# Performance work log

Hardware: AMD Instinct MI355X
Metric: run time of the kernel (lower is better)

Reference implementation:

```python
import jax, jax.numpy as jnp
import numpy as np

B, T, C, H = 256, 256, 384, 6
HS = C // H        # 64 head size
P = int(C * 0.8)   # 307 pca_dim
EPS = 1e-6


def _rmsnorm(x, scale):
    rms = jnp.sqrt(jnp.mean(x * x, axis=-1, keepdims=True) + EPS)
    return x / rms * scale


def _orth(W):
    # torch.svd returns V (not V^T); u @ v.t() == u @ vt
    u, _, vt = jnp.linalg.svd(W, full_matrices=False)
    return u @ vt


def setup_inputs() -> dict:
    key = jax.random.key(0)
    ks = jax.random.split(key, 16)
    s = 0.02
    inp = {
        'x': jax.random.normal(ks[0], (B, T, C), jnp.float32),
        'Wq': jax.random.normal(ks[1], (H, C, HS), jnp.float32) * s,
        'Wk': jax.random.normal(ks[2], (H, C, HS), jnp.float32) * s,
        'Wv': jax.random.normal(ks[3], (H, C, HS), jnp.float32) * s,
        'Wp': jax.random.normal(ks[4], (H * HS, C), jnp.float32) * s,
        'bp': jnp.zeros((C,), jnp.float32),
        'scale1': jnp.ones((C,), jnp.float32),
        'scale2': jnp.ones((C,), jnp.float32),
        'W1': jax.random.normal(ks[5], (C, P), jnp.float32) * s,
        'b1': jnp.zeros((P,), jnp.float32),
        'W2': jax.random.normal(ks[6], (P, C), jnp.float32) * s,
        'b2': jnp.zeros((C,), jnp.float32),
        'Wo_in': jax.random.normal(ks[7], (C, C), jnp.float32),
        'Wo_out': jax.random.normal(ks[8], (C, C), jnp.float32),
    }
    return inp


def reference(x, Wq, Wk, Wv, Wp, bp, scale1, scale2, W1, b1, W2, b2, Wo_in, Wo_out):
    # ln1
    h = _rmsnorm(x, scale1)                                   # [B,T,C]
    # multi-head causal self-attention (heads batched via einsum)
    q = jnp.einsum('btc,hcd->bhtd', h, Wq)                    # [B,H,T,HS]
    k = jnp.einsum('btc,hcd->bhtd', h, Wk)
    v = jnp.einsum('btc,hcd->bhtd', h, Wv)
    wei = jnp.einsum('bhtd,bhsd->bhts', q, k) * (HS ** -0.5)  # [B,H,T,T]
    causal = jnp.tril(jnp.ones((T, T), bool))
    wei = jnp.where(causal, wei, -jnp.inf)
    wei = jax.nn.softmax(wei, axis=-1)
    attn = jnp.einsum('bhts,bhsd->bhtd', wei, v)              # [B,H,T,HS]
    attn = attn.transpose(0, 2, 1, 3).reshape(B, T, H * HS)   # concat heads
    h = attn @ Wp + bp + h                                    # residual on ln1 output
    # ln2
    h = _rmsnorm(h, scale2)
    # input orthogonal transform
    h = h @ _orth(Wo_in)
    # PCA feed-forward (dropout = identity in eval)
    h = jax.nn.relu(h @ W1 + b1)
    h = h @ W2 + b2
    # output orthogonal transform + residual on ff output
    out = h @ _orth(Wo_out) + h
    return out
```

## Files before the change

### kernel.cpp

```cpp
#include <hip/hip_runtime.h>

typedef unsigned short u16;
typedef unsigned int   u32;
typedef short s16x8 __attribute__((ext_vector_type(8)));
typedef float f32x4 __attribute__((ext_vector_type(4)));

static __device__ __forceinline__ float bf2f(u16 v){ return __uint_as_float(((u32)v)<<16); }
static __device__ __forceinline__ u16 f2bf(float f){
  u32 u = __float_as_uint(f);
  u32 r = (u + 0x7fffu + ((u>>16)&1u)) >> 16;
  return (u16)r;
}
static __device__ __forceinline__ float cvt(float v){ return v; }
static __device__ __forceinline__ float cvt(u16 v){ return bf2f(v); }
static __device__ __forceinline__ void stv(float* p, float v){ *p = v; }
static __device__ __forceinline__ void stv(u16* p, float v){ *p = f2bf(v); }

static __device__ __forceinline__ void ld2(const float* p, float& a, float& b){
  float2 t = *(const float2*)p; a=t.x; b=t.y;
}
static __device__ __forceinline__ void ld2(const u16* p, float& a, float& b){
  u32 t = *(const u32*)p; a = __uint_as_float(t<<16); b = __uint_as_float(t & 0xffff0000u);
}
static __device__ __forceinline__ void st2(float* p, float a, float b){
  float2 t; t.x=a; t.y=b; *(float2*)p = t;
}
static __device__ __forceinline__ void st2(u16* p, float a, float b){
  *(u32*)p = ((u32)f2bf(a)) | (((u32)f2bf(b))<<16);
}

template<typename TI, typename TO>
__global__ __launch_bounds__(256) void rms_k(const TI* __restrict__ X,
                                             const float* __restrict__ scale,
                                             TO* __restrict__ O)
{
  int row = blockIdx.x*4 + (threadIdx.x>>6);
  int lane = threadIdx.x&63;
  const TI* xr = X + (size_t)row*384;
  float v[6]; float ss = 0.f;
#pragma unroll
  for(int i=0;i<3;i++){
    ld2(xr + 2*lane + 128*i, v[2*i], v[2*i+1]);
    ss += v[2*i]*v[2*i] + v[2*i+1]*v[2*i+1];
  }
#pragma unroll
  for(int off=32; off>0; off>>=1) ss += __shfl_down(ss, off, 64);
  ss = __shfl(ss, 0, 64);
  float r = rsqrtf(ss*(1.0f/384.0f)+1e-6f);
  TO* orow = O + (size_t)row*384;
#pragma unroll
  for(int i=0;i<3;i++){
    int c = 2*lane + 128*i;
    st2(orow + c, v[2*i]*r*scale[c], v[2*i+1]*r*scale[c+1]);
  }
}

__global__ __launch_bounds__(256) void tcast_k(const float* __restrict__ In, long isz,
                                               u16* __restrict__ Out, long osz,
                                               int Rr, int Cc, int ldo)
{
  __shared__ float t[32][33];
  const int z = blockIdx.z;
  const float* I = In + (long)z*isz;
  u16* Oz = Out + (long)z*osz;
  const int r0 = blockIdx.x*32, c0 = blockIdx.y*32;
  const int tx = threadIdx.x&31, ty = threadIdx.x>>5;
#pragma unroll
  for(int rr=ty; rr<32; rr+=8){
    int r = r0+rr, c = c0+tx;
    t[rr][tx] = (r<Rr && c<Cc) ? I[(size_t)r*Cc + c] : 0.f;
  }
  __syncthreads();
#pragma unroll
  for(int cc=ty; cc<32; cc+=8){
    int c = c0+cc, r = r0+tx;
    if(c<Cc && r<ldo) Oz[(size_t)c*ldo + r] = f2bf(t[tx][cc]);
  }
}

template<int NF, typename TC, typename TR>
__global__ __launch_bounds__(256,2) void mgemmN_k(
    const u16* __restrict__ A, int lda,
    const u16* __restrict__ Bt, int ldb,
    TC* __restrict__ C, long cs_hi, int cs_lo, int csz,
    const TR* __restrict__ R,
    const float* __restrict__ bias,
    int N, int Nstore, int K, float beta, int relu, int nby)
{
  constexpr int BN = NF*32;
  __shared__ __align__(16) u16 As[128*40];
  __shared__ __align__(16) u16 Bs[BN*40];
  const int d = blockIdx.x;
  const int xcd = d&7, slot = d>>3;
  const int bm = xcd*64 + slot/nby;
  const int bn = slot - (slot/nby)*nby;
  const int m0 = bm*128, n0 = bn*BN;
  const int tid = threadIdx.x;
  const int w = tid>>6, lane = tid&63;
  const int g4 = lane>>4, l16 = lane&15;
  const int wr = w>>1, wc = w&1;
  const int arow = tid>>1, akc = (tid&1)*16;

  f32x4 fz = {0.f,0.f,0.f,0.f};
  f32x4 acc[4][NF];
#pragma unroll
  for(int i=0;i<4;i++)
#pragma unroll
    for(int j=0;j<NF;j++) acc[i][j]=fz;

  for(int k0=0;k0<K;k0+=32){
    {
      const u16* ga = &A[(size_t)(m0+arow)*lda + k0 + akc];
      uint4 a0 = *(const uint4*)ga;
      uint4 a1 = *(const uint4*)(ga+8);
      *(uint4*)&As[arow*40 + akc]     = a0;
      *(uint4*)&As[arow*40 + akc + 8] = a1;
    }
#pragma unroll
    for(int j=0;j<(BN+127)/128;j++){
      int brow = (tid>>1) + 128*j;
      if(brow < BN){
        int gn = n0 + brow;
        uint4 b0 = make_uint4(0,0,0,0), b1 = b0;
        if(gn < N){
          const u16* gb = &Bt[(size_t)gn*ldb + k0 + akc];
          b0 = *(const uint4*)gb;
          b1 = *(const uint4*)(gb+8);
        }
        *(uint4*)&Bs[brow*40 + akc]     = b0;
        *(uint4*)&Bs[brow*40 + akc + 8] = b1;
      }
    }
    __syncthreads();
    s16x8 av[4];
#pragma unroll
    for(int mf=0;mf<4;mf++)
      av[mf] = *(const s16x8*)&As[(wr*64 + mf*16 + l16)*40 + g4*8];
#pragma unroll
    for(int nf=0;nf<NF;nf++){
      s16x8 bv = *(const s16x8*)&Bs[(wc*(NF*16) + nf*16 + l16)*40 + g4*8];
#pragma unroll
      for(int mf=0;mf<4;mf++)
        acc[mf][nf] = __builtin_amdgcn_mfma_f32_16x16x32_bf16(av[mf], bv, acc[mf][nf], 0,0,0);
    }
    __syncthreads();
  }
#pragma unroll
  for(int mf=0;mf<4;mf++)
#pragma unroll
    for(int i=0;i<4;i++){
      int m = m0 + wr*64 + mf*16 + g4*4 + i;
      long rowoff = (long)(m>>8)*cs_hi + (long)(m&255)*cs_lo;
#pragma unroll
      for(int nf=0;nf<NF;nf++){
        int gn = n0 + wc*(NF*16) + nf*16 + l16;
        if(gn < Nstore){
          long addr = rowoff + (long)(gn>>6)*csz + (gn&63);
          float v = 0.f;
          if(gn < N){
            v = acc[mf][nf][i];
            if(R)    v += beta*cvt(R[addr]);
            if(bias) v += bias[gn];
            if(relu) v  = fmaxf(v, 0.f);
          }
          stv(C + addr, v);
        }
      }
    }
}

__global__ __launch_bounds__(256,2) void mattn_k(const u16* __restrict__ QKV,
                                                 u16* __restrict__ O)
{
  __shared__ __align__(16) u16 Ks[64*64];
  __shared__ __align__(16) u16 Vts[64*64];
  __shared__ __align__(16) u16 Ps[4*4096];
  const int bh = blockIdx.x;
  const int b = bh/6, h = bh - b*6;
  const u16* Qb = QKV + (size_t)bh*49152;
  const u16* Kb = Qb + 16384;
  const u16* Vb = Qb + 32768;
  const int tid = threadIdx.x;
  const int w = tid>>6, lane = tid&63;
  const int g4 = lane>>4, l16 = lane&15;
  char* PB = (char*)&Ps[w*4096];
  const int swz = (l16&7)<<4;

  s16x8 qf[4][2];
#pragma unroll
  for(int mi=0;mi<4;mi++)
#pragma unroll
    for(int ks=0;ks<2;ks++)
      qf[mi][ks] = *(const s16x8*)(Qb + (size_t)(w*64 + mi*16 + l16)*64 + ks*32 + g4*8);

  f32x4 fzv = {0.f,0.f,0.f,0.f};
  f32x4 o[4][4];
#pragma unroll
  for(int mf=0;mf<4;mf++)
#pragma unroll
    for(int df=0;df<4;df++) o[mf][df]=fzv;
  float mrun[4], lrun[4];
#pragma unroll
  for(int mi=0;mi<4;mi++){ mrun[mi]=-1e30f; lrun[mi]=0.f; }

  for(int st=0; st<4; ++st){
    if(st) __syncthreads();
#pragma unroll
    for(int it=0; it<2; ++it){
      int c = tid + 256*it;
      int s = c>>3, d0 = (c&7)*8;
      uint4 ld = *(const uint4*)(Kb + (size_t)(st*64+s)*64 + d0);
      int byte = s*128 + d0*2; byte ^= (s&7)<<4;
      *(uint4*)((char*)Ks + byte) = ld;
    }
#pragma unroll
    for(int it=0; it<2; ++it){
      int c = tid + 256*it;
      int s = c&63, d0 = (c>>6)*8;
      uint4 ld = *(const uint4*)(Vb + (size_t)(st*64+s)*64 + d0);
#pragma unroll
      for(int jj=0; jj<4; ++jj){
        u32 ww = (jj==0)?ld.x:(jj==1)?ld.y:(jj==2)?ld.z:ld.w;
        int d = d0 + 2*jj;
        int byte0 = d*128 + s*2;     byte0 ^= (d&7)<<4;
        int byte1 = (d+1)*128 + s*2; byte1 ^= ((d+1)&7)<<4;
        *(u16*)((char*)Vts + byte0) = (u16)(ww & 0xffffu);
        *(u16*)((char*)Vts + byte1) = (u16)(ww >> 16);
      }
    }
    __syncthreads();
    if(w < st) continue;

    f32x4 sc[4][4];
#pragma unroll
    for(int sf=0; sf<4; ++sf){
      int row = sf*16 + l16;
      s16x8 kf0 = *(const s16x8*)((char*)Ks + ((row*128 + g4*16) ^ swz));
      s16x8 kf1 = *(const s16x8*)((char*)Ks + ((row*128 + 64 + g4*16) ^ swz));
#pragma unroll
      for(int mi=0; mi<4; ++mi){
        f32x4 t = __builtin_amdgcn_mfma_f32_16x16x32_bf16(kf0, qf[mi][0], fzv, 0,0,0);
        sc[sf][mi] = __builtin_amdgcn_mfma_f32_16x16x32_bf16(kf1, qf[mi][1], t, 0,0,0);
      }
    }
    float alpha[4];
#pragma unroll
    for(int mi=0; mi<4; ++mi){
      int mloc = mi*16 + l16;
      float rmax = -3.0e38f;
#pragma unroll
      for(int sf=0; sf<4; ++sf)
#pragma unroll
        for(int i=0;i<4;i++){
          float vv = sc[sf][mi][i]*0.125f;
          if(st==w && (sf*16 + g4*4 + i) > mloc) vv = -1e30f;
          sc[sf][mi][i] = vv;
          rmax = fmaxf(rmax, vv);
        }
      rmax = fmaxf(rmax, __shfl_xor(rmax, 16, 64));
      rmax = fmaxf(rmax, __shfl_xor(rmax, 32, 64));
      float mnew = fmaxf(mrun[mi], rmax);
      float al = __expf(mrun[mi] - mnew);
      mrun[mi] = mnew;
      float ls = 0.f;
#pragma unroll
      for(int sf=0; sf<4; ++sf){
        float p0 = __expf(sc[sf][mi][0]-mnew);
        float p1 = __expf(sc[sf][mi][1]-mnew);
        float p2 = __expf(sc[sf][mi][2]-mnew);
        float p3 = __expf(sc[sf][mi][3]-mnew);
        ls += p0+p1+p2+p3;
        ushort4 pk; pk.x=f2bf(p0); pk.y=f2bf(p1); pk.z=f2bf(p2); pk.w=f2bf(p3);
        int byte = mloc*128 + sf*32 + g4*8; byte ^= (l16&7)<<4;
        *(ushort4*)(PB + byte) = pk;
      }
      ls += __shfl_xor(ls, 16, 64);
      ls += __shfl_xor(ls, 32, 64);
      lrun[mi] = lrun[mi]*al + ls;
      alpha[mi] = al;
    }
#pragma unroll
    for(int mf=0; mf<4; ++mf)
#pragma unroll
      for(int i=0;i<4;i++){
        float at = __shfl(alpha[mf], g4*4 + i, 64);
#pragma unroll
        for(int df=0; df<4; ++df) o[mf][df][i] *= at;
      }
    s16x8 vbf[4][2];
#pragma unroll
    for(int df=0; df<4; ++df){
      int row = df*16 + l16;
      vbf[df][0] = *(const s16x8*)((char*)Vts + ((row*128 + g4*16) ^ swz));
      vbf[df][1] = *(const s16x8*)((char*)Vts + ((row*128 + 64 + g4*16) ^ swz));
    }
#pragma unroll
    for(int mf=0; mf<4; ++mf){
      int row = mf*16 + l16;
      s16x8 pa0 = *(const s16x8*)(PB + ((row*128 + g4*16) ^ swz));
      s16x8 pa1 = *(const s16x8*)(PB + ((row*128 + 64 + g4*16) ^ swz));
#pragma unroll
      for(int df=0; df<4; ++df){
        f32x4 t = __builtin_amdgcn_mfma_f32_16x16x32_bf16(pa0, vbf[df][0], o[mf][df], 0,0,0);
        o[mf][df] = __builtin_amdgcn_mfma_f32_16x16x32_bf16(pa1, vbf[df][1], t, 0,0,0);
      }
    }
  }
#pragma unroll
  for(int mf=0; mf<4; ++mf)
#pragma unroll
    for(int i=0;i<4;i++){
      float lt = __shfl(lrun[mf], g4*4 + i, 64);
      float rl = 1.f/lt;
      u16* orow = O + ((size_t)(b*256 + w*64 + mf*16 + g4*4 + i))*384 + h*64;
#pragma unroll
      for(int df=0; df<4; ++df)
        orow[df*16 + l16] = f2bf(o[mf][df][i]*rl);
    }
}

__global__ __launch_bounds__(256) void fpart_k(const float* __restrict__ W0,
                                               const float* __restrict__ W1,
                                               float* __restrict__ part)
{
  int b = blockIdx.x; int z = b/24, seg = b - z*24;
  const float* W = (z ? W1 : W0) + seg*6144;
  int tid = threadIdx.x;
  float s = 0.f;
  for(int i=tid;i<6144;i+=256){ float v=W[i]; s+=v*v; }
#pragma unroll
  for(int off=32; off>0; off>>=1) s += __shfl_down(s, off, 64);
  __shared__ float red[4];
  if((tid&63)==0) red[tid>>6]=s;
  __syncthreads();
  if(tid==0) part[b] = red[0]+red[1]+red[2]+red[3];
}

__global__ __launch_bounds__(64) void fcomb_k(const float* __restrict__ part,
                                              float* __restrict__ invb)
{
  int lane = threadIdx.x;
  float v = 0.f;
  if(lane < 24) v = part[lane];
  else if(lane >= 32 && lane < 56) v = part[lane - 8];
#pragma unroll
  for(int off=1; off<32; off<<=1) v += __shfl_xor(v, off, 64);
  if(lane==0)  invb[0] = rsqrtf(v);
  if(lane==32) invb[1] = rsqrtf(v);
}

__global__ __launch_bounds__(256) void nsinit_k(const float* __restrict__ W0,
                                                const float* __restrict__ W1,
                                                const float* __restrict__ invb,
                                                u16* __restrict__ XB)
{
  int b = blockIdx.x; int z = b/24, p = b - z*24, cp0 = p*16;
  const float* W = z ? W1 : W0;
  float inv = invb[z];
  u16* base = XB + (size_t)z*589824;
  u16* xh = base;            u16* xl = base + 147456;
  u16* th = base + 294912;   u16* tl = base + 442368;
  int tid = threadIdx.x;
  for(int idx=tid; idx<6144; idx+=256){
    int r = idx>>4, j = idx&15;
    float v = W[r*384 + cp0 + j]*inv;
    u16 hh = f2bf(v);
    xh[p*6144 + idx] = hh;
    xl[p*6144 + idx] = f2bf(v - bf2f(hh));
  }
  for(int idx=tid; idx<6144; idx+=256){
    int j = idx/384, r = idx - j*384;
    float v = W[(cp0+j)*384 + r]*inv;
    u16 hh = f2bf(v);
    th[p*6144 + r*16 + j] = hh;
    tl[p*6144 + r*16 + j] = f2bf(v - bf2f(hh));
  }
}

static __device__ __forceinline__ void ns_mm(
    const u16* __restrict__ Agh, const u16* __restrict__ Agl,
    u16* AhL, u16* AlL, const u16* BThL, const u16* BTlL,
    int tid, f32x4 acc[4])
{
  const int w = tid>>6, lane = tid&63, g4 = lane>>4, l16 = lane&15;
  const int o0 = (tid>>1)*24 + (tid&1)*8;
  const int o1 = o0 + 4608;
  const s16x8 z8 = {0,0,0,0,0,0,0,0};
  f32x4 fz = {0.f,0.f,0.f,0.f};
#pragma unroll
  for(int i=0;i<4;i++) acc[i]=fz;
  {
    uint4 h0 = *(const uint4*)(Agh + tid*8);
    uint4 h1 = *(const uint4*)(Agh + (384+tid)*8);
    uint4 l0 = *(const uint4*)(Agl + tid*8);
    uint4 l1 = *(const uint4*)(Agl + (384+tid)*8);
    *(uint4*)&AhL[o0] = h0; *(uint4*)&AhL[o1] = h1;
    *(uint4*)&AlL[o0] = l0; *(uint4*)&AlL[o1] = l1;
  }
  __syncthreads();
  for(int c=0;c<24;c++){
    uint4 nh0, nh1, nl0, nl1;
    if(c<23){
      const u16* ph = Agh + (c+1)*6144;
      const u16* pl = Agl + (c+1)*6144;
      nh0 = *(const uint4*)(ph + tid*8);
      nh1 = *(const uint4*)(ph + (384+tid)*8);
      nl0 = *(const uint4*)(pl + tid*8);
      nl1 = *(const uint4*)(pl + (384+tid)*8);
    }
    s16x8 bh = z8, bl = z8;
    if(g4<2){
      bh = *(const s16x8*)&BThL[l16*392 + c*16 + g4*8];
      bl = *(const s16x8*)&BTlL[l16*392 + c*16 + g4*8];
    }
#pragma unroll
    for(int tt=0;tt<4;tt++){
      int rb = 64*w + 16*tt + l16;
      s16x8 ah = z8, al = z8;
      if(g4<2){
        ah = *(const s16x8*)&AhL[rb*24 + g4*8];
        al = *(const s16x8*)&AlL[rb*24 + g4*8];
      }
      acc[tt] = __builtin_amdgcn_mfma_f32_16x16x32_bf16(ah, bh, acc[tt], 0,0,0);
      acc[tt] = __builtin_amdgcn_mfma_f32_16x16x32_bf16(ah, bl, acc[tt], 0,0,0);
      acc[tt] = __builtin_amdgcn_mfma_f32_16x16x32_bf16(al, bh, acc[tt], 0,0,0);
    }
    __syncthreads();
    if(c<23){
      *(uint4*)&AhL[o0] = nh0; *(uint4*)&AhL[o1] = nh1;
      *(uint4*)&AlL[o0] = nl0; *(uint4*)&AlL[o1] = nl1;
      __syncthreads();
    }
  }
}

__global__ __launch_bounds__(384) void nsit_k(u16* __restrict__ XB,
                                              u16* __restrict__ QT,
                                              int it, int niter, int nq)
{
  __shared__ __align__(16) u16 AhL[384*24];
  __shared__ __align__(16) u16 AlL[384*24];
  __shared__ __align__(16) u16 BTh[16*392];
  __shared__ __align__(16) u16 BTl[16*392];
  const int blk = blockIdx.x;
  const int z = blk/24, p = blk - z*24, cp0 = p*16;
  const int tid = threadIdx.x;
  const int w = tid>>6, lane = tid&63, g4 = lane>>4, l16 = lane&15;
  const int rs = it&1, ws2 = rs^1;
  const u16* bin  = XB + (size_t)rs*1179648  + (size_t)z*589824;
  u16*       bout = XB + (size_t)ws2*1179648 + (size_t)z*589824;
  const u16* Xh  = bin;            const u16* Xl  = bin + 147456;
  const u16* Th  = bin + 294912;   const u16* Tl  = bin + 442368;

  {
    const u16* sh = Xh + p*6144;
    const u16* sl = Xl + p*6144;
    for(int i=tid; i<768; i+=384){
      int k = i>>1, n0 = (i&1)*8;
      uint4 vh = *(const uint4*)(sh + i*8);
      uint4 vl = *(const uint4*)(sl + i*8);
#pragma unroll
      for(int j=0;j<8;j++){
        BTh[(n0+j)*392 + k] = ((u16*)&vh)[j];
        BTl[(n0+j)*392 + k] = ((u16*)&vl)[j];
      }
    }
  }
  __syncthreads();

  const bool quint = (it < nq);
  f32x4 acc[4], gsv[4];

  ns_mm(Th, Tl, AhL, AlL, BTh, BTl, tid, acc);
  if(quint){
#pragma unroll
    for(int tt=0;tt<4;tt++){
      gsv[tt] = acc[tt];
      int m0 = 64*w + 16*tt + g4*4;
      ushort4 h4, l4;
#pragma unroll
      for(int i=0;i<4;i++){
        float v = acc[tt][i];
        u16 hh = f2bf(v);
        ((u16*)&h4)[i]=hh; ((u16*)&l4)[i]=f2bf(v - bf2f(hh));
      }
      *(ushort4*)&BTh[l16*392 + m0] = h4;
      *(ushort4*)&BTl[l16*392 + m0] = l4;
    }
    __syncthreads();
    ns_mm(Xh, Xl, AhL, AlL, BTh, BTl, tid, acc);
#pragma unroll
    for(int tt=0;tt<4;tt++){
      int m0 = 64*w + 16*tt + g4*4;
      ushort4 h4, l4;
#pragma unroll
      for(int i=0;i<4;i++){
        float v = acc[tt][i];
        u16 hh = f2bf(v);
        ((u16*)&h4)[i]=hh; ((u16*)&l4)[i]=f2bf(v - bf2f(hh));
      }
      *(ushort4*)&BTh[l16*392 + m0] = h4;
      *(ushort4*)&BTl[l16*392 + m0] = l4;
    }
    __syncthreads();
    ns_mm(Th, Tl, AhL, AlL, BTh, BTl, tid, acc);
    __syncthreads();
#pragma unroll
    for(int tt=0;tt<4;tt++){
      int m0 = 64*w + 16*tt + g4*4;
      ushort4 gh = *(const ushort4*)&BTh[l16*392 + m0];
      ushort4 gl = *(const ushort4*)&BTl[l16*392 + m0];
      (void)gh; (void)gl;
      ushort4 h4, l4;
#pragma unroll
      for(int i=0;i<4;i++){
        float v = fmaf(2.0315f, acc[tt][i], -4.7750f*(gsv[tt][i]))
                + ((m0+i)==(cp0+l16) ? 3.4445f : 0.f);
        u16 hh = f2bf(v);
        ((u16*)&h4)[i]=hh; ((u16*)&l4)[i]=f2bf(v - bf2f(hh));
      }
      *(ushort4*)&BTh[l16*392 + m0] = h4;
      *(ushort4*)&BTl[l16*392 + m0] = l4;
    }
    __syncthreads();
  } else {
#pragma unroll
    for(int tt=0;tt<4;tt++){
      int m0 = 64*w + 16*tt + g4*4;
      ushort4 h4, l4;
#pragma unroll
      for(int i=0;i<4;i++){
        float v = -0.5f*acc[tt][i] + ((m0+i)==(cp0+l16) ? 1.5f : 0.f);
        u16 hh = f2bf(v);
        ((u16*)&h4)[i]=hh; ((u16*)&l4)[i]=f2bf(v - bf2f(hh));
      }
      *(ushort4*)&BTh[l16*392 + m0] = h4;
      *(ushort4*)&BTl[l16*392 + m0] = l4;
    }
    __syncthreads();
  }
  ns_mm(Xh, Xl, AhL, AlL, BTh, BTl, tid, acc);

  if(it == niter-1){
    u16* q = QT + (size_t)z*147456 + (size_t)(cp0+l16)*384;
#pragma unroll
    for(int tt=0;tt<4;tt++){
      int m0 = 64*w + 16*tt + g4*4;
      ushort4 h4;
#pragma unroll
      for(int i=0;i<4;i++) ((u16*)&h4)[i] = f2bf(acc[tt][i]);
      *(ushort4*)&q[m0] = h4;
    }
  } else {
    u16* oXh = bout + p*6144;            u16* oXl = bout + 147456 + p*6144;
    u16* oTh = bout + 294912;            u16* oTl = bout + 442368;
#pragma unroll
    for(int tt=0;tt<4;tt++){
      int m0 = 64*w + 16*tt + g4*4;
      ushort4 h4, l4;
#pragma unroll
      for(int i=0;i<4;i++){
        float v = acc[tt][i];
        u16 hh = f2bf(v);
        ((u16*)&h4)[i]=hh; ((u16*)&l4)[i]=f2bf(v - bf2f(hh));
        oXh[(m0+i)*16 + l16] = hh;
        oXl[(m0+i)*16 + l16] = ((u16*)&l4)[i];
      }
      size_t to = (size_t)(4*w+tt)*6144 + (size_t)(cp0+l16)*16 + g4*4;
      *(ushort4*)&oTh[to] = h4;
      *(ushort4*)&oTl[to] = l4;
    }
  }
}

extern "C" void kernel_launch(void* const* d_in, const int* in_sizes, int n_in,
                              void* d_out, int out_size, void* d_ws, size_t ws_size,
                              hipStream_t stream)
{
  const float* x      = (const float*)d_in[0];
  const float* Wq     = (const float*)d_in[1];
  const float* Wk     = (const float*)d_in[2];
  const float* Wv     = (const float*)d_in[3];
  const float* Wp     = (const float*)d_in[4];
  const float* bp     = (const float*)d_in[5];
  const float* scale1 = (const float*)d_in[6];
  const float* scale2 = (const float*)d_in[7];
  const float* W1     = (const float*)d_in[8];
  const float* b1     = (const float*)d_in[9];
  const float* W2     = (const float*)d_in[10];
  const float* b2     = (const float*)d_in[11];
  const float* Wo_in  = (const float*)d_in[12];
  const float* Wo_out = (const float*)d_in[13];

  char* ws = (char*)d_ws;
  u16* XB   = (u16*)(ws + 0);
  u16* Wqkv = (u16*)(ws + 4719104L);
  u16* WpT  = (u16*)(ws + 5603840L);
  u16* W1T  = (u16*)(ws + 5898752L);
  u16* W2T  = (u16*)(ws + 6134528L);
  u16* QT   = (u16*)(ws + 6380288L);
  float* part = (float*)(ws + 6970112L);
  float* invb = (float*)(ws + 6970496L);
  u16* h1b  = (u16*)(ws + 8388608L);
  u16* qkvb = (u16*)(ws + 58720256L);
  u16* atb  = (u16*)(ws + 209715200L);
  u16* h2b = qkvb;
  u16* h3b = qkvb + 25165824L;
  u16* h4b = qkvb + 50331648L;
  u16* h5b = atb;
  u16* h6b = h1b;

  tcast_k<<<dim3(12, 2,6),256,0,stream>>>(Wq,24576L, Wqkv,        73728L, 384, 64,384);
  tcast_k<<<dim3(12, 2,6),256,0,stream>>>(Wk,24576L, Wqkv+24576L, 73728L, 384, 64,384);
  tcast_k<<<dim3(12, 2,6),256,0,stream>>>(Wv,24576L, Wqkv+49152L, 73728L, 384, 64,384);
  tcast_k<<<dim3(12,12,1),256,0,stream>>>(Wp,0L,     WpT,0L,     384,384,384);
  tcast_k<<<dim3(12,10,1),256,0,stream>>>(W1,0L,     W1T,0L,     384,307,384);
  tcast_k<<<dim3(10,12,1),256,0,stream>>>(W2,0L,     W2T,0L,     307,384,320);

  const int NITER = 15, NQ = 10;
  fpart_k<<<48,256,0,stream>>>(Wo_in, Wo_out, part);
  fcomb_k<<<1,64,0,stream>>>(part, invb);
  nsinit_k<<<48,256,0,stream>>>(Wo_in, Wo_out, invb, XB);
  for(int it=0; it<NITER; ++it)
    nsit_k<<<48,384,0,stream>>>(XB, QT, it, NITER, NQ);

  rms_k<float,u16><<<16384,256,0,stream>>>(x, scale1, h1b);
  mgemmN_k<12,u16,float><<<1536,256,0,stream>>>(
      h1b,384,  Wqkv,384,
      qkvb, 294912L,64,16384,
      (const float*)nullptr, nullptr,
      1152,1152,384, 0.f,0, 3);
  mattn_k<<<1536,256,0,stream>>>(qkvb, atb);
  mgemmN_k<12,u16,u16><<<512,256,0,stream>>>(
      atb,384,  WpT,384,
      h2b, 98304L,384,64,
      h1b, bp,
      384,384,384, 1.f,0, 1);
  rms_k<u16,u16><<<16384,256,0,stream>>>(h2b, scale2, h3b);
  mgemmN_k<12,u16,float><<<512,256,0,stream>>>(
      h3b,384,  QT,384,
      h4b, 98304L,384,64,
      (const float*)nullptr, nullptr,
      384,384,384, 0.f,0, 1);
  mgemmN_k<10,u16,float><<<512,256,0,stream>>>(
      h4b,384,  W1T,384,
      h5b, 81920L,320,64,
      (const float*)nullptr, b1,
      307,320,384, 0.f,1, 1);
  mgemmN_k<12,u16,float><<<512,256,0,stream>>>(
      h5b,320,  W2T,320,
      h6b, 98304L,384,64,
      (const float*)nullptr, b2,
      384,384,320, 0.f,0, 1);
  mgemmN_k<12,float,u16><<<512,256,0,stream>>>(
      h6b,384,  QT+147456,384,
      (float*)d_out, 98304L,384,64,
      h6b, nullptr,
      384,384,384, 1.f,0, 1);

  (void)in_sizes; (void)n_in; (void)ws_size; (void)out_size;
}
```

Measured before the change: 1.700 ms.

## Rewrite bf16 MFMA GEMM with direct global-to-LDS loads and XOR swizzle

The tiled GEMM now loads A and B tiles straight into shared memory with 16-byte global_load_lds instructions instead of staging them through registers. It uses a 64-wide K step with an XOR-swizzled LDS layout, in place of the padded 40-stride layout, to avoid bank conflicts. N tiles are halved, the grids doubled and launch bounds raised to 3 blocks per CU to improve occupancy and overlap. A pair of unused LDS reads in the Newton-Schulz kernel is also dropped. The trade-off is dropping the explicit N bounds guard on B loads, so padded weight rows beyond N are read unchecked (their results are masked at store).

Measured after the change: 1.595 ms. -6.2%, faster.

```diff
diff --git a/kernel.cpp b/kernel.cpp
--- a/kernel.cpp
+++ b/kernel.cpp
@@ -27,6 +27,12 @@
 }
 static __device__ __forceinline__ void st2(u16* p, float a, float b){
   *(u32*)p = ((u32)f2bf(a)) | (((u32)f2bf(b))<<16);
+}
+
+static __device__ __forceinline__ void gload16(const u16* g, u16* l){
+  __builtin_amdgcn_global_load_lds(
+      (const __attribute__((address_space(1))) u32*)(const void*)g,
+      (__attribute__((address_space(3))) u32*)(void*)l, 16, 0, 0);
 }
 
 template<typename TI, typename TO>
@@ -79,7 +85,7 @@
 }
 
 template<int NF, typename TC, typename TR>
-__global__ __launch_bounds__(256,2) void mgemmN_k(
+__global__ __launch_bounds__(256,3) void mgemm2_k(
     const u16* __restrict__ A, int lda,
     const u16* __restrict__ Bt, int ldb,
     TC* __restrict__ C, long cs_hi, int cs_lo, int csz,
@@ -88,8 +94,8 @@
     int N, int Nstore, int K, float beta, int relu, int nby)
 {
   constexpr int BN = NF*32;
-  __shared__ __align__(16) u16 As[128*40];
-  __shared__ __align__(16) u16 Bs[BN*40];
+  __shared__ __align__(16) u16 As[128*64];
+  __shared__ __align__(16) u16 Bs[BN*64];
   const int d = blockIdx.x;
   const int xcd = d&7, slot = d>>3;
   const int bm = xcd*64 + slot/nby;
@@ -99,7 +105,16 @@
   const int w = tid>>6, lane = tid&63;
   const int g4 = lane>>4, l16 = lane&15;
   const int wr = w>>1, wc = w&1;
-  const int arow = tid>>1, akc = (tid&1)*16;
+  const int srow = lane>>3;
+  const int sc8  = ((lane&7) ^ srow) * 8;
+  const u16* aSrc[4];
+#pragma unroll
+  for(int i=0;i<4;i++)
+    aSrc[i] = A + (size_t)(m0 + 8*(w+4*i) + srow)*lda + sc8;
+  const u16* bSrc[NF];
+#pragma unroll
+  for(int i=0;i<NF;i++)
+    bSrc[i] = Bt + (size_t)(n0 + 8*(w+4*i) + srow)*ldb + sc8;
 
   f32x4 fz = {0.f,0.f,0.f,0.f};
   f32x4 acc[4][NF];
@@ -108,40 +123,32 @@
 #pragma unroll
     for(int j=0;j<NF;j++) acc[i][j]=fz;
 
-  for(int k0=0;k0<K;k0+=32){
-    {
-      const u16* ga = &A[(size_t)(m0+arow)*lda + k0 + akc];
-      uint4 a0 = *(const uint4*)ga;
-      uint4 a1 = *(const uint4*)(ga+8);
-      *(uint4*)&As[arow*40 + akc]     = a0;
-      *(uint4*)&As[arow*40 + akc + 8] = a1;
-    }
-#pragma unroll
-    for(int j=0;j<(BN+127)/128;j++){
-      int brow = (tid>>1) + 128*j;
-      if(brow < BN){
-        int gn = n0 + brow;
-        uint4 b0 = make_uint4(0,0,0,0), b1 = b0;
-        if(gn < N){
-          const u16* gb = &Bt[(size_t)gn*ldb + k0 + akc];
-          b0 = *(const uint4*)gb;
-          b1 = *(const uint4*)(gb+8);
-        }
-        *(uint4*)&Bs[brow*40 + akc]     = b0;
-        *(uint4*)&Bs[brow*40 + akc + 8] = b1;
-      }
-    }
-    __syncthreads();
-    s16x8 av[4];
-#pragma unroll
-    for(int mf=0;mf<4;mf++)
-      av[mf] = *(const s16x8*)&As[(wr*64 + mf*16 + l16)*40 + g4*8];
-#pragma unroll
-    for(int nf=0;nf<NF;nf++){
-      s16x8 bv = *(const s16x8*)&Bs[(wc*(NF*16) + nf*16 + l16)*40 + g4*8];
+  const int sxor = l16&7;
+  for(int k0=0;k0<K;k0+=64){
+#pragma unroll
+    for(int i=0;i<4;i++)  gload16(aSrc[i] + k0, &As[(w+4*i)*512]);
+#pragma unroll
+    for(int i=0;i<NF;i++) gload16(bSrc[i] + k0, &Bs[(w+4*i)*512]);
+    __syncthreads();
+#pragma unroll
+    for(int ks=0; ks<2; ++ks){
+      s16x8 av[4];
+#pragma unroll
+      for(int mf=0;mf<4;mf++){
+        int Rr_ = wr*64 + mf*16 + l16;
+        av[mf] = *(const s16x8*)&As[Rr_*64 + 8*((ks*4+g4) ^ sxor)];
+      }
+      s16x8 bv[NF];
+#pragma unroll
+      for(int nf=0;nf<NF;nf++){
+        int Rn = wc*(NF*16) + nf*16 + l16;
+        bv[nf] = *(const s16x8*)&Bs[Rn*64 + 8*((ks*4+g4) ^ sxor)];
+      }
 #pragma unroll
       for(int mf=0;mf<4;mf++)
-        acc[mf][nf] = __builtin_amdgcn_mfma_f32_16x16x32_bf16(av[mf], bv, acc[mf][nf], 0,0,0);
+#pragma unroll
+        for(int nf=0;nf<NF;nf++)
+          acc[mf][nf] = __builtin_amdgcn_mfma_f32_16x16x32_bf16(av[mf], bv[nf], acc[mf][nf], 0,0,0);
     }
     __syncthreads();
   }
@@ -508,9 +515,6 @@
 #pragma unroll
     for(int tt=0;tt<4;tt++){
       int m0 = 64*w + 16*tt + g4*4;
-      ushort4 gh = *(const ushort4*)&BTh[l16*392 + m0];
-      ushort4 gl = *(const ushort4*)&BTl[l16*392 + m0];
-      (void)gh; (void)gl;
       ushort4 h4, l4;
 #pragma unroll
       for(int i=0;i<4;i++){
@@ -625,38 +629,38 @@
     nsit_k<<<48,384,0,stream>>>(XB, QT, it, NITER, NQ);
 
   rms_k<float,u16><<<16384,256,0,stream>>>(x, scale1, h1b);
-  mgemmN_k<12,u16,float><<<1536,256,0,stream>>>(
+  mgemm2_k<6,u16,float><<<3072,256,0,stream>>>(
       h1b,384,  Wqkv,384,
       qkvb, 294912L,64,16384,
       (const float*)nullptr, nullptr,
-      1152,1152,384, 0.f,0, 3);
+      1152,1152,384, 0.f,0, 6);
   mattn_k<<<1536,256,0,stream>>>(qkvb, atb);
-  mgemmN_k<12,u16,u16><<<512,256,0,stream>>>(
+  mgemm2_k<6,u16,u16><<<1024,256,0,stream>>>(
       atb,384,  WpT,384,
       h2b, 98304L,384,64,
       h1b, bp,
-      384,384,384, 1.f,0, 1);
+      384,384,384, 1.f,0, 2);
   rms_k<u16,u16><<<16384,256,0,stream>>>(h2b, scale2, h3b);
-  mgemmN_k<12,u16,float><<<512,256,0,stream>>>(
+  mgemm2_k<6,u16,float><<<1024,256,0,stream>>>(
       h3b,384,  QT,384,
       h4b, 98304L,384,64,
       (const float*)nullptr, nullptr,
-      384,384,384, 0.f,0, 1);
-  mgemmN_k<10,u16,float><<<512,256,0,stream>>>(
+      384,384,384, 0.f,0, 2);
+  mgemm2_k<5,u16,float><<<1024,256,0,stream>>>(
       h4b,384,  W1T,384,
       h5b, 81920L,320,64,
       (const float*)nullptr, b1,
-      307,320,384, 0.f,1, 1);
-  mgemmN_k<12,u16,float><<<512,256,0,stream>>>(
+      307,320,384, 0.f,1, 2);
+  mgemm2_k<6,u16,float><<<1024,256,0,stream>>>(
       h5b,320,  W2T,320,
       h6b, 98304L,384,64,
       (const float*)nullptr, b2,
-      384,384,320, 0.f,0, 1);
-  mgemmN_k<12,float,u16><<<512,256,0,stream>>>(
+      384,384,320, 0.f,0, 2);
+  mgemm2_k<6,float,u16><<<1024,256,0,stream>>>(
       h6b,384,  QT+147456,384,
       (float*)d_out, 98304L,384,64,
       h6b, nullptr,
-      384,384,384, 1.f,0, 1);
+      384,384,384, 1.f,0, 2);
 
   (void)in_sizes; (void)n_in; (void)ws_size; (void)out_size;
 }
```
